# Performance work log

Hardware: AMD Instinct MI355X
Metric: run time of the kernel (lower is better)

The kernel has to match this reference:

```python
import jax, jax.numpy as jnp
import numpy as np

N = 4096
IN_F = 256
OUT_F = 64
HEADS = 4
EDGE_F = 32
ALPHA = 0.2  # leaky relu negative slope


def setup_inputs() -> dict:
    key = jax.random.key(0)
    k1, k2, k3, k4, k5 = jax.random.split(key, 5)
    h = jax.random.normal(k1, (N, IN_F), dtype=jnp.float32)
    adj = jax.random.randint(k2, (N, N, 1), 0, 2, dtype=jnp.int32)
    edge_attr = jax.random.normal(k3, (N, EDGE_F), dtype=jnp.float32)
    # xavier-uniform-ish params
    W = jax.random.normal(k4, (IN_F, HEADS * OUT_F), dtype=jnp.float32) * 0.1
    a = jax.random.normal(k5, (HEADS, 2 * OUT_F + EDGE_F, 1), dtype=jnp.float32) * 0.1
    return {"h": h, "adj": adj, "edge_attr": edge_attr, "W": W, "a": a}


def reference(h, adj, edge_attr, W, a):
    n = h.shape[0]
    Wh = (h @ W).reshape(n, HEADS, OUT_F)            # [N, H, O]
    a_vec = a[:, :, 0]                               # [H, 2O+E]
    a_src = a_vec[:, :OUT_F]                         # [H, O]
    a_dst = a_vec[:, OUT_F:2 * OUT_F]                # [H, O]
    a_edge = a_vec[:, 2 * OUT_F:]                    # [H, E]
    # decompose the all-pairs concat dot-product: score(i,j,h) =
    #   a_src.Wh[i] + a_dst.Wh[j] + a_edge.edge_attr[j]  (edge term follows repeat(N,1) semantics)
    src = jnp.einsum('nho,ho->nh', Wh, a_src)        # [N, H]
    dst = jnp.einsum('nho,ho->nh', Wh, a_dst)        # [N, H]
    edg = jnp.einsum('ne,he->nh', edge_attr, a_edge) # [N, H]
    e = jax.nn.leaky_relu(src[:, None, :] + (dst + edg)[None, :, :],
                          negative_slope=ALPHA)       # [N, N, H]
    att = jnp.where(adj > 0, e, jnp.zeros((), e.dtype))
    att = jax.nn.softmax(att, axis=1)                # softmax over neighbors j
    # dropout p=0.0 (eval): no-op
    h_prime = jnp.einsum('ijh,jho->iho', att, Wh)    # [N, H, O]
    return jax.nn.elu(h_prime.reshape(n, HEADS * OUT_F))
```

## Files before the change

### kernel.cpp

```cpp
#include <hip/hip_runtime.h>
#include <hip/hip_bf16.h>
#include <math.h>

#define NN 4096
#define IN_F 256
#define OUT_F 64
#define HEADS 4
#define EDGE_F 32
#define HO 256
#define AVEC 160
#define ALPHA 0.2f
#define LOG2E 1.44269504088896f

typedef __attribute__((ext_vector_type(8))) short bf16x8;
typedef __attribute__((ext_vector_type(4))) float f32x4;

__device__ __forceinline__ float exp2fast(float x) {
    return __builtin_amdgcn_exp2f(x);
}

__device__ __forceinline__ unsigned short f2bf(float x) {
    unsigned u = __float_as_uint(x);
    u += 0x7FFF + ((u >> 16) & 1);
    return (unsigned short)(u >> 16);
}

__global__ __launch_bounds__(256) void k_pack(const int* __restrict__ adj,
                                              unsigned* __restrict__ abitsT) {
    const int i = blockIdx.x;
    const int w = threadIdx.x >> 6, l = threadIdx.x & 63;
    const int* row = adj + (size_t)i * NN + w * 1024;
#pragma unroll
    for (int r = 0; r < 16; ++r) {
        const unsigned long long m = __ballot(row[r * 64 + l] > 0);
        const int jw = w * 32 + r * 2;
        if (l == 0) abitsT[(size_t)jw * NN + i] = (unsigned)m;
        else if (l == 1) abitsT[(size_t)(jw + 1) * NN + i] = (unsigned)(m >> 32);
    }
}

__global__ __launch_bounds__(256) void k_wh(const float* __restrict__ h,
                                            const float* __restrict__ W,
                                            const float* __restrict__ a,
                                            const float* __restrict__ edge_attr,
                                            unsigned short* __restrict__ pk,
                                            float* __restrict__ src,
                                            float* __restrict__ cdpT) {
    __shared__ float hs[32][32];
    __shared__ float Ws[32][64];
    const int jb = blockIdx.x >> 2, hd = blockIdx.x & 3;
    const int n0 = jb * 32;
    const int tid = threadIdx.x;
    const int rg = tid >> 6, cl = tid & 63;
    float acc[8];
#pragma unroll
    for (int r = 0; r < 8; ++r) acc[r] = 0.f;

    for (int kc = 0; kc < IN_F; kc += 32) {
        {
            const int r = tid >> 3, k4 = (tid & 7) << 2;
            *(float4*)&hs[r][k4] = *(const float4*)&h[(size_t)(n0 + r) * IN_F + kc + k4];
        }
#pragma unroll
        for (int q = 0; q < 2; ++q) {
            const int f = tid + q * 256;
            const int k = f >> 4, c4 = (f & 15) << 2;
            *(float4*)&Ws[k][c4] = *(const float4*)&W[(size_t)(kc + k) * HO + hd * 64 + c4];
        }
        __syncthreads();
#pragma unroll
        for (int k = 0; k < 32; ++k) {
            const float wv = Ws[k][cl];
#pragma unroll
            for (int r = 0; r < 8; ++r)
                acc[r] = fmaf(hs[rg * 8 + r][k], wv, acc[r]);
        }
        __syncthreads();
    }

    {
        const int g = cl >> 4, lr = cl & 15;
        unsigned short* fb = pk + ((size_t)(jb * HEADS + hd) * 4 + g) * 512;
        bf16x8 v;
#pragma unroll
        for (int r = 0; r < 8; ++r) v[r] = (short)f2bf(acc[r]);
        *(bf16x8*)(fb + (rg * 16 + lr) * 8) = v;
    }

    const float asrc = a[hd * AVEC + cl];
    const float adst = a[hd * AVEC + OUT_F + cl];
    float s_keep = 0.f, d_keep = 0.f;
#pragma unroll
    for (int r = 0; r < 8; ++r) {
        float sp = acc[r] * asrc;
        float dp = acc[r] * adst;
#pragma unroll
        for (int off = 32; off >= 1; off >>= 1) {
            sp += __shfl_xor(sp, off);
            dp += __shfl_xor(dp, off);
        }
        if (cl == r) { s_keep = sp; d_keep = dp; }
    }
    if (cl < 8) {
        const int i = n0 + rg * 8 + cl;
        float eg = 0.f;
        const float* erow = edge_attr + (size_t)i * EDGE_F;
#pragma unroll
        for (int e4 = 0; e4 < EDGE_F; e4 += 4) {
            const float4 ev = *(const float4*)(erow + e4);
            const float4 av = *(const float4*)(a + hd * AVEC + 2 * OUT_F + e4);
            eg = fmaf(ev.x, av.x, fmaf(ev.y, av.y, fmaf(ev.z, av.z, fmaf(ev.w, av.w, eg))));
        }
        src[i * HEADS + hd] = s_keep * LOG2E;
        cdpT[(size_t)hd * NN + i] = (d_keep + eg) * LOG2E;
    }
}

__global__ __launch_bounds__(512, 4) void k_pv(const unsigned* __restrict__ abitsT,
                                               const unsigned short* __restrict__ pk,
                                               const float* __restrict__ src,
                                               const float* __restrict__ cdpT,
                                               float* __restrict__ out) {
    __shared__ float plds[4][32][65];
    __shared__ float lsum[4][32];
    const int tid = threadIdx.x;
    const int w = tid >> 6, l = tid & 63;
    const int js = w & 3, mt = w >> 2;
    const int ib = blockIdx.x >> 2, hd = blockIdx.x & 3;
    const int i0 = ib * 32;
    const int lr = l & 15, kb = l >> 4;
    const int i = i0 + mt * 16 + lr;
    const float si = src[i * HEADS + hd];
    const float* crow = cdpT + (size_t)hd * NN + kb * 8;
    const unsigned short* pkb = pk + (size_t)hd * 2048 + l * 8;

    f32x4 acc0 = {0.f, 0.f, 0.f, 0.f};
    f32x4 acc1 = {0.f, 0.f, 0.f, 0.f};
    f32x4 acc2 = {0.f, 0.f, 0.f, 0.f};
    f32x4 acc3 = {0.f, 0.f, 0.f, 0.f};
    float Ls = 0.f;

    for (int jt = js * 32; jt < NN; jt += 128) {
        const unsigned wbits = abitsT[(size_t)(jt >> 5) * NN + i];
        const unsigned byte = (wbits >> (kb * 8)) & 0xFFu;
        const float4 c0 = *(const float4*)(crow + jt);
        const float4 c1 = *(const float4*)(crow + jt + 4);
        const unsigned short* fb = pkb + (size_t)(jt >> 5) * (HEADS * 4 * 512);
        const bf16x8 b0 = *(const bf16x8*)(fb);
        const bf16x8 b1 = *(const bf16x8*)(fb + 512);
        const bf16x8 b2 = *(const bf16x8*)(fb + 1024);
        const bf16x8 b3 = *(const bf16x8*)(fb + 1536);
        float e, p0, p1, p2, p3, p4, p5, p6, p7;
        e = si + c0.x; e = fmaxf(e, ALPHA * e); e = (byte &   1u) ? e : 0.f; p0 = exp2fast(e);
        e = si + c0.y; e = fmaxf(e, ALPHA * e); e = (byte &   2u) ? e : 0.f; p1 = exp2fast(e);
        e = si + c0.z; e = fmaxf(e, ALPHA * e); e = (byte &   4u) ? e : 0.f; p2 = exp2fast(e);
        e = si + c0.w; e = fmaxf(e, ALPHA * e); e = (byte &   8u) ? e : 0.f; p3 = exp2fast(e);
        e = si + c1.x; e = fmaxf(e, ALPHA * e); e = (byte &  16u) ? e : 0.f; p4 = exp2fast(e);
        e = si + c1.y; e = fmaxf(e, ALPHA * e); e = (byte &  32u) ? e : 0.f; p5 = exp2fast(e);
        e = si + c1.z; e = fmaxf(e, ALPHA * e); e = (byte &  64u) ? e : 0.f; p6 = exp2fast(e);
        e = si + c1.w; e = fmaxf(e, ALPHA * e); e = (byte & 128u) ? e : 0.f; p7 = exp2fast(e);
        Ls += ((p0 + p1) + (p2 + p3)) + ((p4 + p5) + (p6 + p7));
        bf16x8 af;
        af[0] = (short)f2bf(p0); af[1] = (short)f2bf(p1);
        af[2] = (short)f2bf(p2); af[3] = (short)f2bf(p3);
        af[4] = (short)f2bf(p4); af[5] = (short)f2bf(p5);
        af[6] = (short)f2bf(p6); af[7] = (short)f2bf(p7);
        acc0 = __builtin_amdgcn_mfma_f32_16x16x32_bf16(af, b0, acc0, 0, 0, 0);
        acc1 = __builtin_amdgcn_mfma_f32_16x16x32_bf16(af, b1, acc1, 0, 0, 0);
        acc2 = __builtin_amdgcn_mfma_f32_16x16x32_bf16(af, b2, acc2, 0, 0, 0);
        acc3 = __builtin_amdgcn_mfma_f32_16x16x32_bf16(af, b3, acc3, 0, 0, 0);
    }

    Ls += __shfl_xor(Ls, 16);
    Ls += __shfl_xor(Ls, 32);
    if (l < 16) lsum[js][mt * 16 + lr] = Ls;
#pragma unroll
    for (int r = 0; r < 4; ++r) {
        const int row = mt * 16 + kb * 4 + r;
        plds[js][row][ 0 + lr] = acc0[r];
        plds[js][row][16 + lr] = acc1[r];
        plds[js][row][32 + lr] = acc2[r];
        plds[js][row][48 + lr] = acc3[r];
    }
    __syncthreads();

    const int row = tid >> 4, c4 = (tid & 15) << 2;
    const float L = lsum[0][row] + lsum[1][row] + lsum[2][row] + lsum[3][row];
    const float inv = 1.f / L;
    float4 o;
    float x;
    x = (plds[0][row][c4 + 0] + plds[1][row][c4 + 0] + plds[2][row][c4 + 0] + plds[3][row][c4 + 0]) * inv;
    o.x = x > 0.f ? x : (__expf(x) - 1.f);
    x = (plds[0][row][c4 + 1] + plds[1][row][c4 + 1] + plds[2][row][c4 + 1] + plds[3][row][c4 + 1]) * inv;
    o.y = x > 0.f ? x : (__expf(x) - 1.f);
    x = (plds[0][row][c4 + 2] + plds[1][row][c4 + 2] + plds[2][row][c4 + 2] + plds[3][row][c4 + 2]) * inv;
    o.z = x > 0.f ? x : (__expf(x) - 1.f);
    x = (plds[0][row][c4 + 3] + plds[1][row][c4 + 3] + plds[2][row][c4 + 3] + plds[3][row][c4 + 3]) * inv;
    o.w = x > 0.f ? x : (__expf(x) - 1.f);
    *(float4*)(out + (size_t)(i0 + row) * HO + hd * 64 + c4) = o;
}

extern "C" void kernel_launch(void* const* d_in, const int* in_sizes, int n_in,
                              void* d_out, int out_size, void* d_ws, size_t ws_size,
                              hipStream_t stream) {
    const float* h         = (const float*)d_in[0];
    const int*   adj       = (const int*)d_in[1];
    const float* edge_attr = (const float*)d_in[2];
    const float* W         = (const float*)d_in[3];
    const float* a         = (const float*)d_in[4];
    float* out = (float*)d_out;

    unsigned short* pk     = (unsigned short*)d_ws;
    float*          cdpT   = (float*)(pk + (size_t)NN * HO);
    float*          src    = cdpT + (size_t)HEADS * NN;
    unsigned*       abitsT = (unsigned*)(src + (size_t)NN * HEADS);

    k_pack<<<NN, 256, 0, stream>>>(adj, abitsT);
    k_wh<<<128 * HEADS, 256, 0, stream>>>(h, W, a, edge_attr, pk, src, cdpT);
    k_pv<<<128 * HEADS, 512, 0, stream>>>(abitsT, pk, src, cdpT, out);
}
```

Baseline: 173.0 us.

## Merge pack and Wh kernels into one launch; compute row sums via MFMA

Folds the adjacency bit-pack kernel and the Wh projection kernel into a single launch, with blocks split by index, so one launch and its inter-kernel gap go away and the two independent jobs can run at the same time. In the attention kernel, the softmax denominator is now taken from an extra MFMA against a vector of bf16 ones rather than from scalar adds plus cross-lane shuffles. This frees VALU work in the hot loop but adds a fifth MFMA per iteration. It also sums the bf16-rounded probabilities, so the denominator now matches the rounded numerator.

```diff
diff --git a/kernel.cpp b/kernel.cpp
--- a/kernel.cpp
+++ b/kernel.cpp
@@ -25,32 +25,33 @@
     return (unsigned short)(u >> 16);
 }
 
-__global__ __launch_bounds__(256) void k_pack(const int* __restrict__ adj,
+__global__ __launch_bounds__(256) void k_prep(const float* __restrict__ h,
+                                              const float* __restrict__ W,
+                                              const float* __restrict__ a,
+                                              const float* __restrict__ edge_attr,
+                                              const int* __restrict__ adj,
+                                              unsigned short* __restrict__ pk,
+                                              float* __restrict__ src,
+                                              float* __restrict__ cdpT,
                                               unsigned* __restrict__ abitsT) {
-    const int i = blockIdx.x;
-    const int w = threadIdx.x >> 6, l = threadIdx.x & 63;
-    const int* row = adj + (size_t)i * NN + w * 1024;
-#pragma unroll
-    for (int r = 0; r < 16; ++r) {
-        const unsigned long long m = __ballot(row[r * 64 + l] > 0);
-        const int jw = w * 32 + r * 2;
-        if (l == 0) abitsT[(size_t)jw * NN + i] = (unsigned)m;
-        else if (l == 1) abitsT[(size_t)(jw + 1) * NN + i] = (unsigned)(m >> 32);
-    }
-}
-
-__global__ __launch_bounds__(256) void k_wh(const float* __restrict__ h,
-                                            const float* __restrict__ W,
-                                            const float* __restrict__ a,
-                                            const float* __restrict__ edge_attr,
-                                            unsigned short* __restrict__ pk,
-                                            float* __restrict__ src,
-                                            float* __restrict__ cdpT) {
+    const int tid = threadIdx.x;
+    if (blockIdx.x >= 512) {
+        const int i = blockIdx.x - 512;
+        const int w = tid >> 6, l = tid & 63;
+        const int* row = adj + (size_t)i * NN + w * 1024;
+#pragma unroll
+        for (int r = 0; r < 16; ++r) {
+            const unsigned long long m = __ballot(row[r * 64 + l] > 0);
+            const int jw = w * 32 + r * 2;
+            if (l == 0) abitsT[(size_t)jw * NN + i] = (unsigned)m;
+            else if (l == 1) abitsT[(size_t)(jw + 1) * NN + i] = (unsigned)(m >> 32);
+        }
+        return;
+    }
     __shared__ float hs[32][32];
     __shared__ float Ws[32][64];
     const int jb = blockIdx.x >> 2, hd = blockIdx.x & 3;
     const int n0 = jb * 32;
-    const int tid = threadIdx.x;
     const int rg = tid >> 6, cl = tid & 63;
     float acc[8];
 #pragma unroll
@@ -134,11 +135,15 @@
     const float* crow = cdpT + (size_t)hd * NN + kb * 8;
     const unsigned short* pkb = pk + (size_t)hd * 2048 + l * 8;
 
+    bf16x8 bones;
+#pragma unroll
+    for (int r = 0; r < 8; ++r) bones[r] = (short)0x3F80;
+
     f32x4 acc0 = {0.f, 0.f, 0.f, 0.f};
     f32x4 acc1 = {0.f, 0.f, 0.f, 0.f};
     f32x4 acc2 = {0.f, 0.f, 0.f, 0.f};
     f32x4 acc3 = {0.f, 0.f, 0.f, 0.f};
-    float Ls = 0.f;
+    f32x4 accL = {0.f, 0.f, 0.f, 0.f};
 
     for (int jt = js * 32; jt < NN; jt += 128) {
         const unsigned wbits = abitsT[(size_t)(jt >> 5) * NN + i];
@@ -159,7 +164,6 @@
         e = si + c1.y; e = fmaxf(e, ALPHA * e); e = (byte &  32u) ? e : 0.f; p5 = exp2fast(e);
         e = si + c1.z; e = fmaxf(e, ALPHA * e); e = (byte &  64u) ? e : 0.f; p6 = exp2fast(e);
         e = si + c1.w; e = fmaxf(e, ALPHA * e); e = (byte & 128u) ? e : 0.f; p7 = exp2fast(e);
-        Ls += ((p0 + p1) + (p2 + p3)) + ((p4 + p5) + (p6 + p7));
         bf16x8 af;
         af[0] = (short)f2bf(p0); af[1] = (short)f2bf(p1);
         af[2] = (short)f2bf(p2); af[3] = (short)f2bf(p3);
@@ -169,11 +173,14 @@
         acc1 = __builtin_amdgcn_mfma_f32_16x16x32_bf16(af, b1, acc1, 0, 0, 0);
         acc2 = __builtin_amdgcn_mfma_f32_16x16x32_bf16(af, b2, acc2, 0, 0, 0);
         acc3 = __builtin_amdgcn_mfma_f32_16x16x32_bf16(af, b3, acc3, 0, 0, 0);
-    }
-
-    Ls += __shfl_xor(Ls, 16);
-    Ls += __shfl_xor(Ls, 32);
-    if (l < 16) lsum[js][mt * 16 + lr] = Ls;
+        accL = __builtin_amdgcn_mfma_f32_16x16x32_bf16(af, bones, accL, 0, 0, 0);
+    }
+
+    if (lr == 0) {
+#pragma unroll
+        for (int r = 0; r < 4; ++r)
+            lsum[js][mt * 16 + kb * 4 + r] = accL[r];
+    }
 #pragma unroll
     for (int r = 0; r < 4; ++r) {
         const int row = mt * 16 + kb * 4 + r;
@@ -215,7 +222,6 @@
     float*          src    = cdpT + (size_t)HEADS * NN;
     unsigned*       abitsT = (unsigned*)(src + (size_t)NN * HEADS);
 
-    k_pack<<<NN, 256, 0, stream>>>(adj, abitsT);
-    k_wh<<<128 * HEADS, 256, 0, stream>>>(h, W, a, edge_attr, pk, src, cdpT);
+    k_prep<<<512 + NN, 256, 0, stream>>>(h, W, a, edge_attr, adj, pk, src, cdpT, abitsT);
     k_pv<<<128 * HEADS, 512, 0, stream>>>(abitsT, pk, src, cdpT, out);
 }
```

Measured after the change: 182.2 us. 5.3% more time.
